# Kernel tuning notes

Hardware: AMD Instinct MI355X
Metric: run time of the kernel (lower is better)

Reference implementation:

```python
import jax, jax.numpy as jnp
import numpy as np

TEMPERATURE = 8.0  # sqrt(d_k), d_k = 64
MINIMUM_VALUE = -1e9  # stand-in for C.MINIMUM_VALUE


def setup_inputs() -> dict:
    key = jax.random.key(0)
    kq, kk, kv, km = jax.random.split(key, 4)
    B, N, D = 32, 2048, 64
    q = jax.random.normal(kq, (B, N, D), dtype=jnp.float32)
    k = jax.random.normal(kk, (B, N, D), dtype=jnp.float32)
    v = jax.random.normal(kv, (B, N, D), dtype=jnp.float32)
    mask = jax.random.randint(km, (B, N, N), 0, 2, dtype=jnp.int32)
    return {"q": q, "k": k, "v": v, "mask": mask}


def reference(q, k, v, mask):
    # scores: [B, Nq, Nk]
    attn = jnp.einsum("bqd,bkd->bqk", q, k) / TEMPERATURE
    attn = jnp.where(mask > 0, attn, MINIMUM_VALUE)
    attn = jax.nn.softmax(attn, axis=-1)
    # dropout is identity in eval / deterministic reference
    output = jnp.einsum("bqk,bkd->bqd", attn, v)
    return (output, attn)
```

## Files before the change

kernel.cpp:

```cpp
#include <hip/hip_runtime.h>

#define NB 32
#define NN 2048
#define ND 64

typedef _Float16 half8 __attribute__((ext_vector_type(8)));
typedef float f32x4 __attribute__((ext_vector_type(4)));

union H4 { uint2 u; _Float16 h[4]; };

__device__ __forceinline__ f32x4 mfma16(half8 a, half8 b, f32x4 c) {
    return __builtin_amdgcn_mfma_f32_16x16x32_f16(a, b, c, 0, 0, 0);
}

__global__ __launch_bounds__(256) void cvt_f32_f16_k(const float* __restrict__ src,
                                                     _Float16* __restrict__ dst) {
    int i = blockIdx.x * 256 + threadIdx.x;
    const f32x4* s = (const f32x4*)src;
    f32x4 a = s[2 * i], b = s[2 * i + 1];
    half8 h;
    h[0] = (_Float16)a[0]; h[1] = (_Float16)a[1]; h[2] = (_Float16)a[2]; h[3] = (_Float16)a[3];
    h[4] = (_Float16)b[0]; h[5] = (_Float16)b[1]; h[6] = (_Float16)b[2]; h[7] = (_Float16)b[3];
    ((half8*)dst)[i] = h;
}

__global__ __launch_bounds__(256) void transpose_v_k(const float* __restrict__ v,
                                                     _Float16* __restrict__ vt) {
    __shared__ float tile[64][65];
    int b = blockIdx.x >> 5;
    int k0 = (blockIdx.x & 31) * 64;
    int t = threadIdx.x;
    {
        int dc = t & 15, kr = t >> 4;
        const f32x4* vp = (const f32x4*)(v + ((size_t)(b * NN + k0) * ND));
        #pragma unroll
        for (int i = 0; i < 4; ++i) {
            int kk = kr + i * 16;
            f32x4 x = vp[kk * 16 + dc];
            tile[kk][dc * 4 + 0] = x[0]; tile[kk][dc * 4 + 1] = x[1];
            tile[kk][dc * 4 + 2] = x[2]; tile[kk][dc * 4 + 3] = x[3];
        }
    }
    __syncthreads();
    {
        int d = t >> 2, ks = (t & 3) * 16;
        union { _Float16 hh[16]; uint4 u4[2]; } pk;
        #pragma unroll
        for (int j = 0; j < 16; ++j) pk.hh[j] = (_Float16)tile[ks + j][d];
        uint4* op = (uint4*)(vt + ((size_t)(b * ND + d) * NN + k0 + ks));
        op[0] = pk.u4[0]; op[1] = pk.u4[1];
    }
}

__global__ __launch_bounds__(256, 1) void attn_main_k(
        const _Float16* __restrict__ qh, const _Float16* __restrict__ kh,
        const _Float16* __restrict__ vt, const int* __restrict__ mask,
        float* __restrict__ outp, float* __restrict__ attnp) {
    extern __shared__ char smem[];

    int bid = blockIdx.x;
    int lin = (bid & 7) * 256 + (bid >> 3);
    int b  = lin >> 6;
    int q0 = (lin & 63) * 32;

    int t = threadIdx.x;
    int w = t >> 6, l = t & 63;
    int l15 = l & 15, lg = l >> 4;

    half8 afr[2][2];
    #pragma unroll
    for (int rb = 0; rb < 2; ++rb)
        #pragma unroll
        for (int ks = 0; ks < 2; ++ks)
            afr[rb][ks] = *(const half8*)(qh +
                ((size_t)(b * NN + q0 + rb * 16 + l15) * ND + ks * 32 + lg * 8));

    const _Float16* kbase = kh + (size_t)b * NN * ND;
    for (int i = 0; i < 32; ++i) {
        int key0 = (w + 4 * i) * 16;
        const _Float16* kp = kbase + (size_t)(key0 + l15) * ND + lg * 8;
        half8 b0 = *(const half8*)kp;
        half8 b1 = *(const half8*)(kp + 32);
        f32x4 acc0 = {0.f, 0.f, 0.f, 0.f};
        f32x4 acc1 = {0.f, 0.f, 0.f, 0.f};
        acc0 = mfma16(afr[0][0], b0, acc0);
        acc0 = mfma16(afr[0][1], b1, acc0);
        acc1 = mfma16(afr[1][0], b0, acc1);
        acc1 = mfma16(afr[1][1], b1, acc1);
        int cb = (key0 + l15) * 2;
        #pragma unroll
        for (int r = 0; r < 4; ++r) {
            int row0 = lg * 4 + r;
            *(_Float16*)(smem + row0 * 4096 + (cb ^ ((row0 & 7) << 4))) =
                (_Float16)(acc0[r] * 0.125f);
            int row1 = row0 + 16;
            *(_Float16*)(smem + row1 * 4096 + (cb ^ ((row1 & 7) << 4))) =
                (_Float16)(acc1[r] * 0.125f);
        }
    }
    __syncthreads();

    int r = t >> 3, g = t & 7;
    char* srow = smem + r * 4096;
    int sw = (r & 7) << 4;
    const int4* mrow = (const int4*)(mask + ((size_t)(b * NN + q0 + r) * NN));
    float mx = -6.0e4f;
    for (int c = 0; c < 8; ++c) {
        int4 mk[8];
        #pragma unroll
        for (int u = 0; u < 8; ++u) mk[u] = mrow[(c * 8 + u) * 8 + g];
        #pragma unroll
        for (int u = 0; u < 8; ++u) {
            int kb = ((((c * 8 + u) * 8 + g) * 4) * 2) ^ sw;
            H4 x; x.u = *(const uint2*)(srow + kb);
            float s0 = mk[u].x > 0 ? (float)x.h[0] : -6.0e4f;
            float s1 = mk[u].y > 0 ? (float)x.h[1] : -6.0e4f;
            float s2 = mk[u].z > 0 ? (float)x.h[2] : -6.0e4f;
            float s3 = mk[u].w > 0 ? (float)x.h[3] : -6.0e4f;
            H4 y;
            y.h[0] = (_Float16)s0; y.h[1] = (_Float16)s1;
            y.h[2] = (_Float16)s2; y.h[3] = (_Float16)s3;
            *(uint2*)(srow + kb) = y.u;
            mx = fmaxf(mx, fmaxf(fmaxf(s0, s1), fmaxf(s2, s3)));
        }
    }
    #pragma unroll
    for (int s = 1; s < 8; s <<= 1) mx = fmaxf(mx, __shfl_xor(mx, s));

    float sum = 0.f;
    for (int c = 0; c < 8; ++c) {
        #pragma unroll
        for (int u = 0; u < 8; ++u) {
            int kb = ((((c * 8 + u) * 8 + g) * 4) * 2) ^ sw;
            H4 x; x.u = *(const uint2*)(srow + kb);
            float p0 = __expf((float)x.h[0] - mx);
            float p1 = __expf((float)x.h[1] - mx);
            float p2 = __expf((float)x.h[2] - mx);
            float p3 = __expf((float)x.h[3] - mx);
            sum += (p0 + p1) + (p2 + p3);
            H4 y;
            y.h[0] = (_Float16)p0; y.h[1] = (_Float16)p1;
            y.h[2] = (_Float16)p2; y.h[3] = (_Float16)p3;
            *(uint2*)(srow + kb) = y.u;
        }
    }
    #pragma unroll
    for (int s = 1; s < 8; s <<= 1) sum += __shfl_xor(sum, s);
    float linv = 1.0f / sum;

    float* arow = attnp + ((size_t)(b * NN + q0 + r) * NN);
    for (int c = 0; c < 8; ++c) {
        #pragma unroll
        for (int u = 0; u < 8; ++u) {
            int k4 = ((c * 8 + u) * 8 + g) * 4;
            int kb = (k4 * 2) ^ sw;
            H4 x; x.u = *(const uint2*)(srow + kb);
            f32x4 av;
            av[0] = (float)x.h[0] * linv;
            av[1] = (float)x.h[1] * linv;
            av[2] = (float)x.h[2] * linv;
            av[3] = (float)x.h[3] * linv;
            *(f32x4*)(arow + k4) = av;
            H4 y;
            y.h[0] = (_Float16)av[0]; y.h[1] = (_Float16)av[1];
            y.h[2] = (_Float16)av[2]; y.h[3] = (_Float16)av[3];
            *(uint2*)(srow + kb) = y.u;
        }
    }
    __syncthreads();

    int rb = w & 1, ct0 = (w >> 1) * 2;
    const _Float16* v0 = vt + (size_t)(b * ND + ct0 * 16 + l15) * NN;
    const _Float16* v1 = v0 + (size_t)16 * NN;
    int arowi = rb * 16 + l15;
    char* abase = smem + arowi * 4096;
    int asw = (arowi & 7) << 4;
    f32x4 o0 = {0.f, 0.f, 0.f, 0.f}, o1 = {0.f, 0.f, 0.f, 0.f};
    for (int ks = 0; ks < 64; ++ks) {
        int kb = (ks * 64 + lg * 16) ^ asw;
        half8 pa  = *(const half8*)(abase + kb);
        half8 vb0 = *(const half8*)(v0 + ks * 32 + lg * 8);
        half8 vb1 = *(const half8*)(v1 + ks * 32 + lg * 8);
        o0 = mfma16(pa, vb0, o0);
        o1 = mfma16(pa, vb1, o1);
    }
    float* ob = outp + ((size_t)(b * NN + q0 + rb * 16 + lg * 4) * ND) + ct0 * 16 + l15;
    #pragma unroll
    for (int rr = 0; rr < 4; ++rr) {
        ob[(size_t)rr * ND]      = o0[rr];
        ob[(size_t)rr * ND + 16] = o1[rr];
    }
}

extern "C" void kernel_launch(void* const* d_in, const int* in_sizes, int n_in,
                              void* d_out, int out_size, void* d_ws, size_t ws_size,
                              hipStream_t stream) {
    const float* q = (const float*)d_in[0];
    const float* k = (const float*)d_in[1];
    const float* v = (const float*)d_in[2];
    const int* mask = (const int*)d_in[3];
    float* outp  = (float*)d_out;
    float* attnp = outp + (size_t)NB * NN * ND;

    _Float16* qh = (_Float16*)d_ws;
    _Float16* kh = qh + (size_t)NB * NN * ND;
    _Float16* vth = kh + (size_t)NB * NN * ND;

    cvt_f32_f16_k<<<2048, 256, 0, stream>>>(q, qh);
    cvt_f32_f16_k<<<2048, 256, 0, stream>>>(k, kh);
    transpose_v_k<<<1024, 256, 0, stream>>>(v, vth);
    attn_main_k<<<2048, 256, 131072, stream>>>(qh, kh, vth, mask, outp, attnp);
}
```

Baseline: 449.3 us.

## Halve rows per block, double threads, keep masked scores in registers

Each block now handles 16 query rows with 512 threads instead of 32 rows with 256 threads. Shared memory per block drops to 64KB, which allows more resident blocks per CU. Masked scores are held in registers across the max, exp and normalize passes, so the shared-memory round trips between passes go away. The P·V product is split into two key halves per wave group and reduced through shared memory. The cost is extra syncs and each K/V tile being reloaded by twice as many blocks.

```diff
diff --git a/kernel.cpp b/kernel.cpp
--- a/kernel.cpp
+++ b/kernel.cpp
@@ -3,6 +3,8 @@
 #define NB 32
 #define NN 2048
 #define ND 64
+#define ROWS 16
+#define NBLK (NB * NN / ROWS)
 
 typedef _Float16 half8 __attribute__((ext_vector_type(8)));
 typedef float f32x4 __attribute__((ext_vector_type(4)));
@@ -52,66 +54,61 @@
     }
 }
 
-__global__ __launch_bounds__(256, 1) void attn_main_k(
+__global__ __launch_bounds__(512, 4) void attn_main_k(
         const _Float16* __restrict__ qh, const _Float16* __restrict__ kh,
         const _Float16* __restrict__ vt, const int* __restrict__ mask,
         float* __restrict__ outp, float* __restrict__ attnp) {
     extern __shared__ char smem[];
 
     int bid = blockIdx.x;
-    int lin = (bid & 7) * 256 + (bid >> 3);
-    int b  = lin >> 6;
-    int q0 = (lin & 63) * 32;
+    int lin = (bid & 7) * (NBLK / 8) + (bid >> 3);
+    int b  = lin >> 7;
+    int q0 = (lin & 127) * ROWS;
 
     int t = threadIdx.x;
     int w = t >> 6, l = t & 63;
     int l15 = l & 15, lg = l >> 4;
 
-    half8 afr[2][2];
-    #pragma unroll
-    for (int rb = 0; rb < 2; ++rb)
-        #pragma unroll
-        for (int ks = 0; ks < 2; ++ks)
-            afr[rb][ks] = *(const half8*)(qh +
-                ((size_t)(b * NN + q0 + rb * 16 + l15) * ND + ks * 32 + lg * 8));
+    half8 afr[2];
+    #pragma unroll
+    for (int ks = 0; ks < 2; ++ks)
+        afr[ks] = *(const half8*)(qh +
+            ((size_t)(b * NN + q0 + l15) * ND + ks * 32 + lg * 8));
 
     const _Float16* kbase = kh + (size_t)b * NN * ND;
-    for (int i = 0; i < 32; ++i) {
-        int key0 = (w + 4 * i) * 16;
+    for (int i = 0; i < 16; ++i) {
+        int key0 = (w + 8 * i) * 16;
         const _Float16* kp = kbase + (size_t)(key0 + l15) * ND + lg * 8;
         half8 b0 = *(const half8*)kp;
         half8 b1 = *(const half8*)(kp + 32);
-        f32x4 acc0 = {0.f, 0.f, 0.f, 0.f};
-        f32x4 acc1 = {0.f, 0.f, 0.f, 0.f};
-        acc0 = mfma16(afr[0][0], b0, acc0);
-        acc0 = mfma16(afr[0][1], b1, acc0);
-        acc1 = mfma16(afr[1][0], b0, acc1);
-        acc1 = mfma16(afr[1][1], b1, acc1);
+        f32x4 acc = {0.f, 0.f, 0.f, 0.f};
+        acc = mfma16(afr[0], b0, acc);
+        acc = mfma16(afr[1], b1, acc);
         int cb = (key0 + l15) * 2;
         #pragma unroll
         for (int r = 0; r < 4; ++r) {
-            int row0 = lg * 4 + r;
-            *(_Float16*)(smem + row0 * 4096 + (cb ^ ((row0 & 7) << 4))) =
-                (_Float16)(acc0[r] * 0.125f);
-            int row1 = row0 + 16;
-            *(_Float16*)(smem + row1 * 4096 + (cb ^ ((row1 & 7) << 4))) =
-                (_Float16)(acc1[r] * 0.125f);
+            int row = lg * 4 + r;
+            *(_Float16*)(smem + row * 4096 + (cb ^ ((row & 7) << 4))) =
+                (_Float16)(acc[r] * 0.125f);
         }
     }
     __syncthreads();
 
-    int r = t >> 3, g = t & 7;
+    int r = t >> 5, g = t & 31;
     char* srow = smem + r * 4096;
     int sw = (r & 7) << 4;
     const int4* mrow = (const int4*)(mask + ((size_t)(b * NN + q0 + r) * NN));
+    uint2 ms[16];
     float mx = -6.0e4f;
-    for (int c = 0; c < 8; ++c) {
+    #pragma unroll
+    for (int c = 0; c < 2; ++c) {
         int4 mk[8];
         #pragma unroll
-        for (int u = 0; u < 8; ++u) mk[u] = mrow[(c * 8 + u) * 8 + g];
+        for (int u = 0; u < 8; ++u) mk[u] = mrow[g + (c * 8 + u) * 32];
         #pragma unroll
         for (int u = 0; u < 8; ++u) {
-            int kb = ((((c * 8 + u) * 8 + g) * 4) * 2) ^ sw;
+            int j = c * 8 + u;
+            int kb = ((g * 4 + j * 128) * 2) ^ sw;
             H4 x; x.u = *(const uint2*)(srow + kb);
             float s0 = mk[u].x > 0 ? (float)x.h[0] : -6.0e4f;
             float s1 = mk[u].y > 0 ? (float)x.h[1] : -6.0e4f;
@@ -120,75 +117,70 @@
             H4 y;
             y.h[0] = (_Float16)s0; y.h[1] = (_Float16)s1;
             y.h[2] = (_Float16)s2; y.h[3] = (_Float16)s3;
-            *(uint2*)(srow + kb) = y.u;
+            ms[j] = y.u;
             mx = fmaxf(mx, fmaxf(fmaxf(s0, s1), fmaxf(s2, s3)));
         }
     }
     #pragma unroll
-    for (int s = 1; s < 8; s <<= 1) mx = fmaxf(mx, __shfl_xor(mx, s));
+    for (int s = 1; s < 32; s <<= 1) mx = fmaxf(mx, __shfl_xor(mx, s));
 
     float sum = 0.f;
-    for (int c = 0; c < 8; ++c) {
-        #pragma unroll
-        for (int u = 0; u < 8; ++u) {
-            int kb = ((((c * 8 + u) * 8 + g) * 4) * 2) ^ sw;
-            H4 x; x.u = *(const uint2*)(srow + kb);
-            float p0 = __expf((float)x.h[0] - mx);
-            float p1 = __expf((float)x.h[1] - mx);
-            float p2 = __expf((float)x.h[2] - mx);
-            float p3 = __expf((float)x.h[3] - mx);
-            sum += (p0 + p1) + (p2 + p3);
-            H4 y;
-            y.h[0] = (_Float16)p0; y.h[1] = (_Float16)p1;
-            y.h[2] = (_Float16)p2; y.h[3] = (_Float16)p3;
-            *(uint2*)(srow + kb) = y.u;
-        }
-    }
-    #pragma unroll
-    for (int s = 1; s < 8; s <<= 1) sum += __shfl_xor(sum, s);
+    #pragma unroll
+    for (int j = 0; j < 16; ++j) {
+        H4 x; x.u = ms[j];
+        float p0 = __expf((float)x.h[0] - mx);
+        float p1 = __expf((float)x.h[1] - mx);
+        float p2 = __expf((float)x.h[2] - mx);
+        float p3 = __expf((float)x.h[3] - mx);
+        sum += (p0 + p1) + (p2 + p3);
+        H4 y;
+        y.h[0] = (_Float16)p0; y.h[1] = (_Float16)p1;
+        y.h[2] = (_Float16)p2; y.h[3] = (_Float16)p3;
+        ms[j] = y.u;
+    }
+    #pragma unroll
+    for (int s = 1; s < 32; s <<= 1) sum += __shfl_xor(sum, s);
     float linv = 1.0f / sum;
 
     float* arow = attnp + ((size_t)(b * NN + q0 + r) * NN);
-    for (int c = 0; c < 8; ++c) {
-        #pragma unroll
-        for (int u = 0; u < 8; ++u) {
-            int k4 = ((c * 8 + u) * 8 + g) * 4;
-            int kb = (k4 * 2) ^ sw;
-            H4 x; x.u = *(const uint2*)(srow + kb);
-            f32x4 av;
-            av[0] = (float)x.h[0] * linv;
-            av[1] = (float)x.h[1] * linv;
-            av[2] = (float)x.h[2] * linv;
-            av[3] = (float)x.h[3] * linv;
-            *(f32x4*)(arow + k4) = av;
-            H4 y;
-            y.h[0] = (_Float16)av[0]; y.h[1] = (_Float16)av[1];
-            y.h[2] = (_Float16)av[2]; y.h[3] = (_Float16)av[3];
-            *(uint2*)(srow + kb) = y.u;
-        }
-    }
-    __syncthreads();
-
-    int rb = w & 1, ct0 = (w >> 1) * 2;
-    const _Float16* v0 = vt + (size_t)(b * ND + ct0 * 16 + l15) * NN;
-    const _Float16* v1 = v0 + (size_t)16 * NN;
-    int arowi = rb * 16 + l15;
-    char* abase = smem + arowi * 4096;
-    int asw = (arowi & 7) << 4;
-    f32x4 o0 = {0.f, 0.f, 0.f, 0.f}, o1 = {0.f, 0.f, 0.f, 0.f};
-    for (int ks = 0; ks < 64; ++ks) {
-        int kb = (ks * 64 + lg * 16) ^ asw;
-        half8 pa  = *(const half8*)(abase + kb);
-        half8 vb0 = *(const half8*)(v0 + ks * 32 + lg * 8);
-        half8 vb1 = *(const half8*)(v1 + ks * 32 + lg * 8);
-        o0 = mfma16(pa, vb0, o0);
-        o1 = mfma16(pa, vb1, o1);
-    }
-    float* ob = outp + ((size_t)(b * NN + q0 + rb * 16 + lg * 4) * ND) + ct0 * 16 + l15;
-    #pragma unroll
-    for (int rr = 0; rr < 4; ++rr) {
-        ob[(size_t)rr * ND]      = o0[rr];
-        ob[(size_t)rr * ND + 16] = o1[rr];
+    #pragma unroll
+    for (int j = 0; j < 16; ++j) {
+        int col = g * 4 + j * 128;
+        H4 x; x.u = ms[j];
+        f32x4 av;
+        av[0] = (float)x.h[0] * linv;
+        av[1] = (float)x.h[1] * linv;
+        av[2] = (float)x.h[2] * linv;
+        av[3] = (float)x.h[3] * linv;
+        *(f32x4*)(arow + col) = av;
+        H4 y;
+        y.h[0] = (_Float16)av[0]; y.h[1] = (_Float16)av[1];
+        y.h[2] = (_Float16)av[2]; y.h[3] = (_Float16)av[3];
+        *(uint2*)(srow + (col * 2 ^ sw)) = y.u;
+    }
+    __syncthreads();
+
+    int ct = w & 3, kseg = w >> 2;
+    const _Float16* vp = vt + (size_t)(b * ND + ct * 16 + l15) * NN + lg * 8;
+    char* abase = smem + l15 * 4096;
+    int asw = (l15 & 7) << 4;
+    f32x4 o = {0.f, 0.f, 0.f, 0.f};
+    #pragma unroll 4
+    for (int kk = 0; kk < 32; ++kk) {
+        int ks = kseg * 32 + kk;
+        half8 pa = *(const half8*)(abase + ((ks * 64 + lg * 16) ^ asw));
+        half8 vb = *(const half8*)(vp + ks * 32);
+        o = mfma16(pa, vb, o);
+    }
+    __syncthreads();
+    if (w >= 4) *(f32x4*)(smem + ((w - 4) * 64 + l) * 16) = o;
+    __syncthreads();
+    if (w < 4) {
+        f32x4 o2 = *(const f32x4*)(smem + (w * 64 + l) * 16);
+        o += o2;
+        float* ob = outp + ((size_t)(b * NN + q0 + lg * 4) * ND) + ct * 16 + l15;
+        #pragma unroll
+        for (int rr = 0; rr < 4; ++rr) ob[(size_t)rr * ND] = o[rr];
     }
 }
 
@@ -209,5 +201,5 @@
     cvt_f32_f16_k<<<2048, 256, 0, stream>>>(q, qh);
     cvt_f32_f16_k<<<2048, 256, 0, stream>>>(k, kh);
     transpose_v_k<<<1024, 256, 0, stream>>>(v, vth);
-    attn_main_k<<<2048, 256, 131072, stream>>>(qh, kh, vth, mask, outp, attnp);
-}
+    attn_main_k<<<NBLK, 512, 65536, stream>>>(qh, kh, vth, mask, outp, attnp);
+}
```

Result: faster. 409.6 us (-8.8%).
